# Performance work log

Measured on AMD Instinct MI355X. Metric: run time of the kernel, lower is better.

Reference implementation:

```python
import jax, jax.numpy as jnp
import numpy as np

N_NODES = 100000
N_EDGES = 1000000
NUM_GRAPHS = 100
EPS_BN = 1e-5
EPS_GATE = 1e-6


def _bn(x, gamma, beta):
    # BatchNorm1d in training mode: batch statistics over dim 0
    mu = jnp.mean(x, axis=0)
    var = jnp.var(x, axis=0)
    return (x - mu) * jax.lax.rsqrt(var + EPS_BN) * gamma + beta


def _gated_gcn_layer(h, e, snorm_n, snorm_e, W, b, g_h, b_h, g_e, b_e, src, dst):
    # W: [5, d, d] stacking A, B, C, D, E projections; b: [5, d]
    Ah = h @ W[0] + b[0]
    Bh = h @ W[1] + b[1]
    Ce = e @ W[2] + b[2]
    Dh = h @ W[3] + b[3]
    Eh = h @ W[4] + b[4]
    # edge update: e_ji = Dh_src + Eh_dst + Ce   [E, d]
    e_new = Dh[src] + Eh[dst] + Ce
    sigma = jax.nn.sigmoid(e_new)
    # node update: gated sum of source messages at destination nodes
    num = jax.ops.segment_sum(sigma * Bh[src], dst, num_segments=h.shape[0])
    den = jax.ops.segment_sum(sigma, dst, num_segments=h.shape[0])
    h_new = Ah + num / (den + EPS_GATE)
    # graph size normalization
    h_new = h_new * snorm_n
    e_new = e_new * snorm_e
    # batch norm + relu + residual (dropout = 0.0)
    h_new = jax.nn.relu(_bn(h_new, g_h, b_h))
    e_new = jax.nn.relu(_bn(e_new, g_e, b_e))
    return h + h_new, e + e_new


def setup_inputs() -> dict:
    key = jax.random.key(0)
    ks = jax.random.split(key, 12)
    nodes_feat = jax.random.normal(ks[0], (N_NODES, 64), jnp.float32)
    edges_feat = jax.random.normal(ks[1], (N_EDGES, 1), jnp.float32)
    snorm_n = jax.random.uniform(ks[2], (N_NODES, 1), jnp.float32)
    snorm_e = jax.random.uniform(ks[3], (N_EDGES, 1), jnp.float32)
    src = jax.random.randint(ks[4], (N_EDGES,), 0, N_NODES, jnp.int32)
    dst = jax.random.randint(ks[5], (N_EDGES,), 0, N_NODES, jnp.int32)
    node_graph_ids = jnp.sort(jax.random.randint(ks[6], (N_NODES,), 0, NUM_GRAPHS, jnp.int32))
    Wh = jax.random.normal(ks[7], (64, 70), jnp.float32) * 0.1
    bh = jnp.zeros((70,), jnp.float32)
    We = jax.random.normal(ks[8], (1, 70), jnp.float32) * 0.1
    be = jnp.zeros((70,), jnp.float32)
    W_gcn = jax.random.normal(ks[9], (3, 5, 70, 70), jnp.float32) * 0.1
    b_gcn = jnp.zeros((3, 5, 70), jnp.float32)
    bn_gamma_h = jnp.ones((3, 70), jnp.float32)
    bn_beta_h = jnp.zeros((3, 70), jnp.float32)
    bn_gamma_e = jnp.ones((3, 70), jnp.float32)
    bn_beta_e = jnp.zeros((3, 70), jnp.float32)
    return {"nodes_feat": nodes_feat, "edges_feat": edges_feat, "snorm_n": snorm_n,
            "snorm_e": snorm_e, "src": src, "dst": dst, "node_graph_ids": node_graph_ids,
            "Wh": Wh, "bh": bh, "We": We, "be": be, "W_gcn": W_gcn, "b_gcn": b_gcn,
            "bn_gamma_h": bn_gamma_h, "bn_beta_h": bn_beta_h,
            "bn_gamma_e": bn_gamma_e, "bn_beta_e": bn_beta_e}


def reference(nodes_feat, edges_feat, snorm_n, snorm_e, src, dst, node_graph_ids,
              Wh, bh, We, be, W_gcn, b_gcn, bn_gamma_h, bn_beta_h, bn_gamma_e, bn_beta_e):
    h = nodes_feat @ Wh + bh
    e = edges_feat @ We + be
    # hidden_dims = [70, 70] -> only gated_gcn_1 (params index 0) and gated_gcn_o (index 2)
    for li in (0, 2):
        h, e = _gated_gcn_layer(h, e, snorm_n, snorm_e, W_gcn[li], b_gcn[li],
                                bn_gamma_h[li], bn_beta_h[li], bn_gamma_e[li], bn_beta_e[li],
                                src, dst)
    # dgl.mean_nodes: per-graph mean of node features
    sums = jax.ops.segment_sum(h, node_graph_ids, num_segments=NUM_GRAPHS)
    counts = jax.ops.segment_sum(jnp.ones((h.shape[0],), h.dtype), node_graph_ids,
                                 num_segments=NUM_GRAPHS)
    hg = sums / jnp.maximum(counts, 1.0)[:, None]
    return hg
```

## Files before the change

### kernel.cpp

```cpp
#include <hip/hip_runtime.h>

#define NN 100000
#define NE 1000000
#define NG 100
#define DD 70
#define EL0 64
#define CH0 (9 * EL0)
#define TPW 5
#define EPW (16 * TPW)
#define EPB (4 * EPW)
#define SCB 512
#define WTS (70 * 72)

typedef __attribute__((ext_vector_type(8))) short bf16x8;
typedef __attribute__((ext_vector_type(4))) float f32x4;

__device__ __forceinline__ float sigmoidf_(float x) { return 1.f / (1.f + expf(-x)); }

__device__ __forceinline__ unsigned int rne_bf16(float x) {
    unsigned int u = __float_as_uint(x);
    return (u + 0x7FFFu + ((u >> 16) & 1u)) >> 16;
}
__device__ __forceinline__ float b2f(unsigned short u) {
    return __uint_as_float(((unsigned int)u) << 16);
}

#define DOT4(acc, vv, ww) { acc = fmaf((vv).x, (ww).x, acc); acc = fmaf((vv).y, (ww).y, acc); \
                            acc = fmaf((vv).z, (ww).z, acc); acc = fmaf((vv).w, (ww).w, acc); }

__global__ void k_trAll(const float* __restrict__ Wh, const float* __restrict__ Wg,
                        float* __restrict__ WT) {
    int m = blockIdx.y, f = blockIdx.x, k = threadIdx.x;
    const float* W;
    int K = DD;
    switch (m) {
        case 0: W = Wh; K = 64; break;
        case 1: W = Wg + 0 * 4900; break;
        case 2: W = Wg + 1 * 4900; break;
        case 3: W = Wg + 3 * 4900; break;
        case 4: W = Wg + 4 * 4900; break;
        case 5: W = Wg + 10 * 4900; break;
        case 6: W = Wg + 11 * 4900; break;
        case 7: W = Wg + 13 * 4900; break;
        default: W = Wg + 14 * 4900; break;
    }
    if (k < 72) WT[(m * 70 + f) * 72 + k] = (k < K) ? W[k * DD + f] : 0.f;
}

__global__ __launch_bounds__(640) void k_dense_r(const float* __restrict__ x, int K,
                                                 const float* __restrict__ WTm,
                                                 const float* __restrict__ bias,
                                                 float* __restrict__ out, int nrows) {
    __shared__ float sx[36 * 72];
    int t = threadIdx.x;
    int r = t / DD, f = t - r * DD;
    long rb = (long)blockIdx.x * 36;
    for (int idx = t; idx < 36 * 72; idx += 640) {
        int rr = idx / 72, kk = idx - rr * 72;
        long i = rb + rr;
        sx[idx] = (kk < K && i < nrows) ? x[i * K + kk] : 0.f;
    }
    __syncthreads();
    if (r < 9) {
        const float4* wr = (const float4*)(WTm + f * 72);
        float bb = bias[f];
        float a0 = bb, a1 = bb, a2 = bb, a3 = bb;
        const float4* s0 = (const float4*)&sx[(r) * 72];
        const float4* s1 = (const float4*)&sx[(r + 9) * 72];
        const float4* s2 = (const float4*)&sx[(r + 18) * 72];
        const float4* s3 = (const float4*)&sx[(r + 27) * 72];
#pragma unroll 1
        for (int q = 0; q < 18; q += 2) {
            float4 wA = wr[q], wB = wr[q + 1];
            float4 vA0 = s0[q], vB0 = s0[q + 1];
            DOT4(a0, vA0, wA) DOT4(a0, vB0, wB)
            float4 vA1 = s1[q], vB1 = s1[q + 1];
            DOT4(a1, vA1, wA) DOT4(a1, vB1, wB)
            float4 vA2 = s2[q], vB2 = s2[q + 1];
            DOT4(a2, vA2, wA) DOT4(a2, vB2, wB)
            float4 vA3 = s3[q], vB3 = s3[q + 1];
            DOT4(a3, vA3, wA) DOT4(a3, vB3, wB)
        }
        long i0 = rb + r, i1 = i0 + 9, i2 = i0 + 18, i3 = i0 + 27;
        if (i0 < nrows) out[i0 * DD + f] = a0;
        if (i1 < nrows) out[i1 * DD + f] = a1;
        if (i2 < nrows) out[i2 * DD + f] = a2;
        if (i3 < nrows) out[i3 * DD + f] = a3;
    }
}

#define PROJ(MIDX, BIAS, STORE)                                                   \
    {                                                                             \
        const float4* wr = (const float4*)(WT4 + (MIDX) * WTS + f * 72);          \
        float bb = (BIAS)[f];                                                     \
        float a0 = bb, a1 = bb, a2 = bb, a3 = bb;                                 \
        _Pragma("unroll 1")                                                       \
        for (int q = 0; q < 18; q += 2) {                                         \
            float4 wA = wr[q], wB = wr[q + 1];                                    \
            float4 vA0 = s0[q], vB0 = s0[q + 1];                                  \
            DOT4(a0, vA0, wA) DOT4(a0, vB0, wB)                                   \
            float4 vA1 = s1[q], vB1 = s1[q + 1];                                  \
            DOT4(a1, vA1, wA) DOT4(a1, vB1, wB)                                   \
            float4 vA2 = s2[q], vB2 = s2[q + 1];                                  \
            DOT4(a2, vA2, wA) DOT4(a2, vB2, wB)                                   \
            float4 vA3 = s3[q], vB3 = s3[q + 1];                                  \
            DOT4(a3, vA3, wA) DOT4(a3, vB3, wB)                                   \
        }                                                                         \
        if (i0 < nrows) STORE(i0, a0);                                            \
        if (i1 < nrows) STORE(i1, a1);                                            \
        if (i2 < nrows) STORE(i2, a2);                                            \
        if (i3 < nrows) STORE(i3, a3);                                            \
    }

__global__ __launch_bounds__(640) void k_dense_q(
    const float* __restrict__ x, const float* __restrict__ WT4,
    const float* __restrict__ bA, const float* __restrict__ bB,
    const float* __restrict__ bD, const float* __restrict__ bE,
    float* __restrict__ outA, unsigned short* __restrict__ outB,
    unsigned short* __restrict__ outD, unsigned short* __restrict__ outE, int nrows) {
    __shared__ float sx[36 * 72];
    int t = threadIdx.x;
    int r = t / DD, f = t - r * DD;
    long rb = (long)blockIdx.x * 36;
    for (int idx = t; idx < 36 * 72; idx += 640) {
        int rr = idx / 72, kk = idx - rr * 72;
        long i = rb + rr;
        sx[idx] = (kk < DD && i < nrows) ? x[i * DD + kk] : 0.f;
    }
    __syncthreads();
    if (r < 9) {
        const float4* s0 = (const float4*)&sx[(r) * 72];
        const float4* s1 = (const float4*)&sx[(r + 9) * 72];
        const float4* s2 = (const float4*)&sx[(r + 18) * 72];
        const float4* s3 = (const float4*)&sx[(r + 27) * 72];
        long i0 = rb + r, i1 = i0 + 9, i2 = i0 + 18, i3 = i0 + 27;
#define ST_A(ii, aa) outA[(ii) * DD + f] = (aa)
#define ST_B(ii, aa) outB[(ii) * DD + f] = (unsigned short)rne_bf16(aa)
#define ST_D(ii, aa) outD[(ii) * DD + f] = (unsigned short)rne_bf16(aa)
#define ST_E(ii, aa) outE[(ii) * DD + f] = (unsigned short)rne_bf16(aa)
        PROJ(0, bA, ST_A)
        PROJ(1, bB, ST_B)
        PROJ(2, bD, ST_D)
        PROJ(3, bE, ST_E)
#undef ST_A
#undef ST_B
#undef ST_D
#undef ST_E
    }
}

__global__ void k_pre(const float* __restrict__ We, const float* __restrict__ be,
                      const float* __restrict__ Wg, const float* __restrict__ bg,
                      float* __restrict__ v1, float* __restrict__ v2) {
    int f = threadIdx.x;
    if (f < DD) {
        const float* W2 = Wg + 2 * DD * DD;
        const float* b2 = bg + 2 * DD;
        float a = 0.f, c = 0.f;
        for (int k = 0; k < DD; ++k) {
            a = fmaf(We[k], W2[k * DD + f], a);
            c = fmaf(be[k], W2[k * DD + f], c);
        }
        v1[f] = a;
        v2[f] = c + b2[f];
    }
}

__global__ void k_prep2(const float* __restrict__ v1, const float* __restrict__ v2,
                        const float* __restrict__ murs_e, const float* __restrict__ ge,
                        const float* __restrict__ bbe, const float* __restrict__ We,
                        const float* __restrict__ be, const float* __restrict__ Wg,
                        float* __restrict__ CT2, unsigned short* __restrict__ WB) {
    int t = threadIdx.x;
    if (t < 35) {
        int f0 = 2 * t, f1 = 2 * t + 1;
        float A0 = murs_e[DD + f0] * ge[f0], A1 = murs_e[DD + f1] * ge[f1];
        float* c = CT2 + t * 12;
        c[0] = v1[f0];  c[1] = v1[f1];
        c[2] = v2[f0];  c[3] = v2[f1];
        c[4] = A0;      c[5] = A1;
        c[6] = bbe[f0] - murs_e[f0] * A0;
        c[7] = bbe[f1] - murs_e[f1] * A1;
        c[8] = We[f0];  c[9] = We[f1];
        c[10] = be[f0]; c[11] = be[f1];
    }
    const float* WC2 = Wg + 12 * 4900;
    for (int idx = t; idx < 960; idx += 512) {
        int nt = idx / 192, rem = idx - nt * 192;
        int c = rem / 64, l = rem - c * 64;
        int n = nt * 16 + (l & 15);
        int kb = c * 32 + (l >> 4) * 8;
        for (int j = 0; j < 8; ++j) {
            int k = kb + j;
            unsigned short v = 0;
            if (k < 70 && n < 70) v = (unsigned short)rne_bf16(WC2[k * 70 + n]);
            WB[((nt * 3 + c) * 64 + l) * 8 + j] = v;
        }
    }
}

__global__ void k_count(const int* __restrict__ dst, int* __restrict__ off) {
    int j = blockIdx.x * 256 + threadIdx.x;
    if (j < NE) atomicAdd(&off[dst[j]], 1);
}

__global__ void k_scan_a(int* __restrict__ off, int* __restrict__ part) {
    __shared__ int s[SCB];
    int t = threadIdx.x, i = blockIdx.x * SCB + t;
    int v = (i < NN) ? off[i] : 0;
    s[t] = v;
    __syncthreads();
    for (int d = 1; d < SCB; d <<= 1) {
        int x = (t >= d) ? s[t - d] : 0;
        __syncthreads();
        s[t] += x;
        __syncthreads();
    }
    if (i < NN) off[i] = s[t] - v;
    if (t == SCB - 1) part[blockIdx.x] = s[t];
}

__global__ void k_scan_b(int* __restrict__ part, int nb) {
    __shared__ int s[256];
    int t = threadIdx.x;
    int v = (t < nb) ? part[t] : 0;
    s[t] = v;
    __syncthreads();
    for (int d = 1; d < 256; d <<= 1) {
        int x = (t >= d) ? s[t - d] : 0;
        __syncthreads();
        s[t] += x;
        __syncthreads();
    }
    if (t < nb) part[t] = s[t] - v;
}

__global__ void k_scan_c(int* __restrict__ off, const int* __restrict__ part) {
    int i = blockIdx.x * SCB + threadIdx.x;
    if (i < NN) off[i] += part[blockIdx.x];
}

__global__ void k_fill(const int* __restrict__ src, const int* __restrict__ dst,
                       const float* __restrict__ ef, const float* __restrict__ sne,
                       int* __restrict__ off, int* __restrict__ src_s,
                       float* __restrict__ ef_s, float* __restrict__ sne_s,
                       int* __restrict__ dst_s) {
    int j = blockIdx.x * 256 + threadIdx.x;
    if (j < NE) {
        int d = dst[j];
        int pos = atomicAdd(&off[d], 1);
        src_s[pos] = src[j];
        ef_s[pos] = ef[j];
        sne_s[pos] = sne[j];
        dst_s[pos] = d;
    }
}

__global__ __launch_bounds__(640) void k_edge0(
    const float* __restrict__ ef_s, const float* __restrict__ sne_s,
    const int* __restrict__ src_s, const int* __restrict__ dst_s,
    const unsigned short* __restrict__ PB, const unsigned short* __restrict__ PD,
    const unsigned short* __restrict__ PE, const float* __restrict__ v1,
    const float* __restrict__ v2, float* __restrict__ num,
    float* __restrict__ den, float* __restrict__ red) {
    int t = threadIdx.x;
    int r = t / DD, f = t - r * DD;
    bool act = (r < 9);
    float c1 = 0.f, c2 = 0.f;
    if (act) { c1 = v1[f]; c2 = v2[f]; }
    float acc_s = 0.f, acc_q = 0.f;
    int e_beg = blockIdx.x * CH0 + r * EL0;
    bool live = act && e_beg < NE;
    int dcur = 0;
    float accn = 0.f, accd = 0.f;
    int lim = 0;
    if (live) {
        dcur = dst_s[e_beg];
        lim = NE - e_beg;
        if (lim > EL0) lim = EL0;
    }
    for (int g = 0; g < lim; g += 4) {
        int m = lim - g;
        if (m > 4) m = 4;
        int dj[4];
        float pdj[4], pbj[4], pej[4], efj[4], snj[4];
#pragma unroll
        for (int j = 0; j < 4; ++j) {
            if (j < m) {
                int e = e_beg + g + j;
                int s = src_s[e];
                int d = dst_s[e];
                dj[j] = d;
                efj[j] = ef_s[e];
                snj[j] = sne_s[e];
                pdj[j] = b2f(PD[(long)s * DD + f]);
                pbj[j] = b2f(PB[(long)s * DD + f]);
                pej[j] = b2f(PE[(long)d * DD + f]);
            }
        }
#pragma unroll
        for (int j = 0; j < 4; ++j) {
            if (j < m) {
                if (dj[j] != dcur) {
                    unsafeAtomicAdd(&num[(long)dcur * DD + f], accn);
                    unsafeAtomicAdd(&den[(long)dcur * DD + f], accd);
                    accn = 0.f; accd = 0.f;
                    dcur = dj[j];
                }
                float en = pdj[j] + pej[j] + efj[j] * c1 + c2;
                float sg = sigmoidf_(en);
                accn = fmaf(sg, pbj[j], accn);
                accd += sg;
                float tv = en * snj[j];
                acc_s += tv;
                acc_q = fmaf(tv, tv, acc_q);
            }
        }
    }
    if (live) {
        unsafeAtomicAdd(&num[(long)dcur * DD + f], accn);
        unsafeAtomicAdd(&den[(long)dcur * DD + f], accd);
    }
    __shared__ float ss[DD], sq[DD];
    if (t < DD) { ss[t] = 0.f; sq[t] = 0.f; }
    __syncthreads();
    if (act) { atomicAdd(&ss[f], acc_s); atomicAdd(&sq[f], acc_q); }
    __syncthreads();
    if (t < DD) {
        atomicAdd(&red[t], ss[t]);
        atomicAdd(&red[DD + t], sq[t]);
    }
}

__global__ __launch_bounds__(256) void k_edge2(
    const float* __restrict__ ef_s, const float* __restrict__ sne_s,
    const int* __restrict__ src_s, const int* __restrict__ dst_s,
    const unsigned short* __restrict__ PD0, const unsigned short* __restrict__ PE0,
    const unsigned short* __restrict__ PB2, const unsigned short* __restrict__ PD2,
    const unsigned short* __restrict__ PE2, const float* __restrict__ CT2,
    const unsigned short* __restrict__ WB, const float* __restrict__ bC2,
    float* __restrict__ num, float* __restrict__ den) {
    __shared__ __align__(16) unsigned short As[4 * 16 * 104];
    int t = threadIdx.x;
    int w = t >> 6, l = t & 63;
    unsigned short* Aw = &As[w * 1664];
    for (int i = l; i < 832; i += 64) ((unsigned int*)Aw)[i] = 0u;
    int wb_e = blockIdx.x * EPB + w * EPW;
    if (wb_e >= NE) return;
    int col = l & 15, hi = l >> 4;
    bf16x8 bfr[15];
#pragma unroll
    for (int q = 0; q < 15; ++q)
        bfr[q] = *(const bf16x8*)(WB + (q * 64 + l) * 8);
    float bc[5];
#pragma unroll
    for (int nt = 0; nt < 5; ++nt) bc[nt] = bC2[nt * 16 + col];
    int e0p = wb_e + hi * 4;
    if (e0p > NE - 1) e0p = NE - 1;
    int dcur = dst_s[e0p];
    float an[5], ad[5];
#pragma unroll
    for (int nt = 0; nt < 5; ++nt) { an[nt] = 0.f; ad[nt] = 0.f; }
    for (int tt = 0; tt < TPW; ++tt) {
        int et = wb_e + tt * 16;
        if (et >= NE) break;
        for (int i = l; i < 560; i += 64) {
            int el = i / 35, fp = i - el * 35, f = fp * 2;
            int e = et + el;
            unsigned int val = 0u;
            if (e < NE) {
                int s = src_s[e], d = dst_s[e];
                float efv = ef_s[e], sn = sne_s[e];
                const float* ct = CT2 + fp * 12;
                unsigned int upd = *(const unsigned int*)(PD0 + (long)s * DD + f);
                unsigned int upe = *(const unsigned int*)(PE0 + (long)d * DD + f);
                float pdx = __uint_as_float(upd << 16);
                float pdy = __uint_as_float(upd & 0xFFFF0000u);
                float pex = __uint_as_float(upe << 16);
                float pey = __uint_as_float(upe & 0xFFFF0000u);
                float en0a = pdx + pex + efv * ct[0] + ct[2];
                float en0b = pdy + pey + efv * ct[1] + ct[3];
                float ra = fmaxf(fmaf(en0a * sn, ct[4], ct[6]), 0.f);
                float rb = fmaxf(fmaf(en0b * sn, ct[5], ct[7]), 0.f);
                float e1a = fmaf(efv, ct[8], ct[10]) + ra;
                float e1b = fmaf(efv, ct[9], ct[11]) + rb;
                val = rne_bf16(e1a) | (rne_bf16(e1b) << 16);
            }
            ((unsigned int*)Aw)[(el * 104 + f) >> 1] = val;
        }
        bf16x8 af[3];
#pragma unroll
        for (int c = 0; c < 3; ++c)
            af[c] = *(const bf16x8*)(Aw + (l & 15) * 104 + c * 32 + hi * 8);
        f32x4 acc[5];
#pragma unroll
        for (int nt = 0; nt < 5; ++nt) {
            acc[nt] = (f32x4){0.f, 0.f, 0.f, 0.f};
#pragma unroll
            for (int c = 0; c < 3; ++c)
                acc[nt] = __builtin_amdgcn_mfma_f32_16x16x32_bf16(af[c], bfr[nt * 3 + c],
                                                                  acc[nt], 0, 0, 0);
        }
#pragma unroll
        for (int j = 0; j < 4; ++j) {
            int e = et + hi * 4 + j;
            if (e < NE) {
                int d = dst_s[e];
                if (d != dcur) {
#pragma unroll
                    for (int nt = 0; nt < 5; ++nt) {
                        int nv = nt * 16 + col;
                        if (nv < 70) {
                            unsafeAtomicAdd(&num[(long)dcur * DD + nv], an[nt]);
                            unsafeAtomicAdd(&den[(long)dcur * DD + nv], ad[nt]);
                        }
                        an[nt] = 0.f; ad[nt] = 0.f;
                    }
                    dcur = d;
                }
                int s = src_s[e];
#pragma unroll
                for (int nt = 0; nt < 5; ++nt) {
                    int nv = nt * 16 + col;
                    if (nv < 70) {
                        float en = acc[nt][j] + bc[nt] + b2f(PD2[(long)s * DD + nv])
                                 + b2f(PE2[(long)d * DD + nv]);
                        float sg = sigmoidf_(en);
                        an[nt] = fmaf(sg, b2f(PB2[(long)s * DD + nv]), an[nt]);
                        ad[nt] += sg;
                    }
                }
            }
        }
    }
#pragma unroll
    for (int nt = 0; nt < 5; ++nt) {
        int nv = nt * 16 + col;
        if (nv < 70) {
            unsafeAtomicAdd(&num[(long)dcur * DD + nv], an[nt]);
            unsafeAtomicAdd(&den[(long)dcur * DD + nv], ad[nt]);
        }
    }
}

__global__ __launch_bounds__(640) void k_nstats(const float* __restrict__ PA,
                                                const float* __restrict__ num,
                                                const float* __restrict__ den,
                                                const float* __restrict__ snn,
                                                float* __restrict__ red) {
    int t = threadIdx.x;
    int r = t / DD, f = t - r * DD;
    bool act = (r < 9);
    float acc_s = 0.f, acc_q = 0.f;
    const int T = (NN + 8) / 9;
    for (int tile = blockIdx.x; tile < T; tile += gridDim.x) {
        int i = tile * 9 + r;
        if (act && i < NN) {
            long o = (long)i * DD + f;
            float v = (PA[o] + num[o] / (den[o] + 1e-6f)) * snn[i];
            acc_s += v;
            acc_q = fmaf(v, v, acc_q);
        }
    }
    __shared__ float ss[DD], sq[DD];
    if (t < DD) { ss[t] = 0.f; sq[t] = 0.f; }
    __syncthreads();
    if (act) { atomicAdd(&ss[f], acc_s); atomicAdd(&sq[f], acc_q); }
    __syncthreads();
    if (t < DD) {
        atomicAdd(&red[t], ss[t]);
        atomicAdd(&red[DD + t], sq[t]);
    }
}

__global__ void k_stats(const float* __restrict__ sums, float* __restrict__ murs, float invn) {
    int f = threadIdx.x;
    if (f < DD) {
        float mu = sums[f] * invn;
        float var = sums[DD + f] * invn - mu * mu;
        murs[f] = mu;
        murs[DD + f] = rsqrtf(var + 1e-5f);
    }
}

__global__ __launch_bounds__(256) void k_apply(const float* __restrict__ hin,
                                               const float* __restrict__ PA,
                                               const float* __restrict__ num,
                                               const float* __restrict__ den,
                                               const float* __restrict__ snn,
                                               const float* __restrict__ murs,
                                               const float* __restrict__ g,
                                               const float* __restrict__ b,
                                               float* __restrict__ hout) {
    long idx = (long)blockIdx.x * 256 + threadIdx.x;
    if (idx < (long)NN * DD) {
        int i = (int)(idx / DD);
        int f = (int)(idx - (long)i * DD);
        float v = (PA[idx] + num[idx] / (den[idx] + 1e-6f)) * snn[i];
        float bnv = (v - murs[f]) * murs[DD + f] * g[f] + b[f];
        hout[idx] = hin[idx] + fmaxf(bnv, 0.f);
    }
}

__global__ __launch_bounds__(640) void k_readout(const float* __restrict__ h,
                                                 const int* __restrict__ gid,
                                                 float* __restrict__ gsum,
                                                 float* __restrict__ gcnt) {
    __shared__ float sv[9 * DD];
    __shared__ int sg_[9];
    int t = threadIdx.x;
    int r = t / DD, f = t - r * DD;
    int i = blockIdx.x * 9 + r;
    if (r < 9 && i < NN) {
        sv[r * DD + f] = h[(long)i * DD + f];
        if (f == 0) sg_[r] = gid[i];
    }
    __syncthreads();
    int nvalid = NN - blockIdx.x * 9;
    if (nvalid > 9) nvalid = 9;
    if (t < DD && nvalid > 0) {
        float acc = 0.f;
        int cur = sg_[0];
        for (int rr = 0; rr < nvalid; ++rr) {
            int g = sg_[rr];
            if (g != cur) {
                unsafeAtomicAdd(&gsum[cur * DD + t], acc);
                acc = 0.f;
                cur = g;
            }
            acc += sv[rr * DD + t];
        }
        unsafeAtomicAdd(&gsum[cur * DD + t], acc);
        if (t == 0) {
            int cnt = 0;
            cur = sg_[0];
            for (int rr = 0; rr < nvalid; ++rr) {
                if (sg_[rr] != cur) {
                    unsafeAtomicAdd(&gcnt[cur], (float)cnt);
                    cnt = 0;
                    cur = sg_[rr];
                }
                cnt++;
            }
            unsafeAtomicAdd(&gcnt[cur], (float)cnt);
        }
    }
}

__global__ void k_out(const float* __restrict__ gsum, const float* __restrict__ gcnt,
                      float* __restrict__ out) {
    int idx = blockIdx.x * 256 + threadIdx.x;
    if (idx < NG * DD) {
        int g = idx / DD;
        out[idx] = gsum[idx] / fmaxf(gcnt[g], 1.f);
    }
}

extern "C" void kernel_launch(void* const* d_in, const int* in_sizes, int n_in,
                              void* d_out, int out_size, void* d_ws, size_t ws_size,
                              hipStream_t stream) {
    const float* x   = (const float*)d_in[0];
    const float* ef  = (const float*)d_in[1];
    const float* snn = (const float*)d_in[2];
    const float* sne = (const float*)d_in[3];
    const int*   src = (const int*)d_in[4];
    const int*   dst = (const int*)d_in[5];
    const int*   gid = (const int*)d_in[6];
    const float* Wh  = (const float*)d_in[7];
    const float* bh  = (const float*)d_in[8];
    const float* We  = (const float*)d_in[9];
    const float* be  = (const float*)d_in[10];
    const float* Wg  = (const float*)d_in[11];
    const float* bg  = (const float*)d_in[12];
    const float* gh  = (const float*)d_in[13];
    const float* bbh = (const float*)d_in[14];
    const float* ge  = (const float*)d_in[15];
    const float* bbe = (const float*)d_in[16];
    float* out = (float*)d_out;

    const size_t NF = (size_t)NN * DD;

    float* ws = (float*)d_ws;
    float* B0 = ws;
    float* B1 = B0 + NF;
    float* B2 = B1 + NF;
    float* B3 = B2 + NF;
    float* B4 = B3 + NF;
    float* B5 = B4 + NF;
    float* B6 = B5 + NF;
    float* num = B6 + NF;
    float* den = num + NF;
    float* red  = den + NF;
    float* gsum = red + 4 * DD;
    float* gcnt = gsum + NG * DD;
    float* v1 = gcnt + NG;
    float* v2 = v1 + DD;
    float* murs_e = v2 + DD;
    float* murs_h = murs_e + 2 * DD;
    int* src_s = (int*)(murs_h + 2 * DD);
    float* ef_s  = (float*)(src_s + NE);
    float* sne_s = ef_s + NE;
    int* dst_s = (int*)(sne_s + NE);
    float* WT    = (float*)(dst_s + NE);
    uintptr_t pal = ((uintptr_t)(WT + 10 * WTS) + 15) & ~(uintptr_t)15;
    float* CT2 = (float*)pal;
    unsigned short* WB = (unsigned short*)(CT2 + 420);
    int* off  = (int*)num;
    int* part = off + NN;

    unsigned short* B0h = (unsigned short*)B0;
    unsigned short* B3h = (unsigned short*)B3;
    unsigned short* B4h = (unsigned short*)B4;
    unsigned short* B5h = (unsigned short*)B5;
    unsigned short* B6h = (unsigned short*)B6;

    size_t need = (size_t)((char*)(WB + 7680) - (char*)d_ws);
    if (ws_size < need) return;

    const int NB_N36 = (NN + 35) / 36;
    const int NB_N9  = (NN + 8) / 9;
    const int NB_E256 = (NE + 255) / 256;
    const int NB_SC  = (NN + SCB - 1) / SCB;
    const int NB_E0  = (NE + CH0 - 1) / CH0;
    const int NB_E2  = (NE + EPB - 1) / EPB;

    hipMemsetAsync(off, 0, NN * sizeof(int), stream);
    k_trAll<<<dim3(70, 9), 72, 0, stream>>>(Wh, Wg, WT);
    k_count<<<NB_E256, 256, 0, stream>>>(dst, off);
    k_scan_a<<<NB_SC, SCB, 0, stream>>>(off, part);
    k_scan_b<<<1, 256, 0, stream>>>(part, NB_SC);
    k_scan_c<<<NB_SC, SCB, 0, stream>>>(off, part);
    k_fill<<<NB_E256, 256, 0, stream>>>(src, dst, ef, sne, off, src_s, ef_s, sne_s, dst_s);

    hipMemsetAsync(num, 0, (2 * NF + 4 * DD + NG * DD + NG) * sizeof(float), stream);

    k_pre<<<1, 128, 0, stream>>>(We, be, Wg, bg, v1, v2);
    k_dense_r<<<NB_N36, 640, 0, stream>>>(x, 64, WT + 0 * WTS, bh, B0, NN);

    k_dense_q<<<NB_N36, 640, 0, stream>>>(B0, WT + 1 * WTS, bg + 0 * 70, bg + 1 * 70,
                                          bg + 3 * 70, bg + 4 * 70, B2, B3h, B4h, B5h, NN);
    k_edge0<<<NB_E0, 640, 0, stream>>>(ef_s, sne_s, src_s, dst_s, B3h, B4h, B5h, v1, v2,
                                       num, den, red);
    k_stats<<<1, 128, 0, stream>>>(red, murs_e, 1.f / NE);
    k_prep2<<<1, 512, 0, stream>>>(v1, v2, murs_e, ge + 0, bbe + 0, We, be, Wg, CT2, WB);
    k_nstats<<<2048, 640, 0, stream>>>(B2, num, den, snn, red + 2 * DD);
    k_stats<<<1, 128, 0, stream>>>(red + 2 * DD, murs_h, 1.f / NN);
    k_apply<<<(int)((NF + 255) / 256), 256, 0, stream>>>(B0, B2, num, den, snn, murs_h,
                                                         gh + 0, bbh + 0, B1);

    hipMemsetAsync(num, 0, (2 * NF + 4 * DD) * sizeof(float), stream);
    k_dense_q<<<NB_N36, 640, 0, stream>>>(B1, WT + 5 * WTS, bg + 10 * 70, bg + 11 * 70,
                                          bg + 13 * 70, bg + 14 * 70, B2, B3h, B0h, B6h, NN);
    k_edge2<<<NB_E2, 256, 0, stream>>>(ef_s, sne_s, src_s, dst_s, B4h, B5h, B3h, B0h, B6h,
                                       CT2, WB, bg + 12 * 70, num, den);
    k_nstats<<<2048, 640, 0, stream>>>(B2, num, den, snn, red + 2 * DD);
    k_stats<<<1, 128, 0, stream>>>(red + 2 * DD, murs_h, 1.f / NN);
    k_apply<<<(int)((NF + 255) / 256), 256, 0, stream>>>(B1, B2, num, den, snn, murs_h,
                                                         gh + 2 * DD, bbh + 2 * DD, B1);

    k_readout<<<NB_N9, 640, 0, stream>>>(B1, gid, gsum, gcnt);
    k_out<<<(NG * DD + 255) / 256, 256, 0, stream>>>(gsum, gcnt, out);
}
```

Measured before the change: 1.707 ms.

## Interleave Dh and Bh as packed bf16 pairs and cache Eh per destination

The dense projection kernel now writes Dh and Bh for each node as one packed 32-bit word, so each edge kernel fetches both source-gathered values with one load instead of two. Because edges are sorted by destination, both edge kernels load Eh[dst] only when the destination changes rather than on every edge. This cuts random gather traffic in the edge-heavy kernels. In exchange, buffer roles are reassigned, and the dense kernel still writes a separate Dh array that later layers reuse, so node-side writes grow somewhat.

```diff
diff --git a/kernel.cpp b/kernel.cpp
--- a/kernel.cpp
+++ b/kernel.cpp
@@ -24,6 +24,8 @@
 __device__ __forceinline__ float b2f(unsigned short u) {
     return __uint_as_float(((unsigned int)u) << 16);
 }
+__device__ __forceinline__ float lo2f(unsigned int u) { return __uint_as_float(u << 16); }
+__device__ __forceinline__ float hi2f(unsigned int u) { return __uint_as_float(u & 0xFFFF0000u); }
 
 #define DOT4(acc, vv, ww) { acc = fmaf((vv).x, (ww).x, acc); acc = fmaf((vv).y, (ww).y, acc); \
                             acc = fmaf((vv).z, (ww).z, acc); acc = fmaf((vv).w, (ww).w, acc); }
@@ -106,18 +108,18 @@
             float4 vA3 = s3[q], vB3 = s3[q + 1];                                  \
             DOT4(a3, vA3, wA) DOT4(a3, vB3, wB)                                   \
         }                                                                         \
-        if (i0 < nrows) STORE(i0, a0);                                            \
-        if (i1 < nrows) STORE(i1, a1);                                            \
-        if (i2 < nrows) STORE(i2, a2);                                            \
-        if (i3 < nrows) STORE(i3, a3);                                            \
+        STORE(0, i0, a0)                                                          \
+        STORE(1, i1, a1)                                                          \
+        STORE(2, i2, a2)                                                          \
+        STORE(3, i3, a3)                                                          \
     }
 
 __global__ __launch_bounds__(640) void k_dense_q(
     const float* __restrict__ x, const float* __restrict__ WT4,
     const float* __restrict__ bA, const float* __restrict__ bB,
     const float* __restrict__ bD, const float* __restrict__ bE,
-    float* __restrict__ outA, unsigned short* __restrict__ outB,
-    unsigned short* __restrict__ outD, unsigned short* __restrict__ outE, int nrows) {
+    float* __restrict__ outA, unsigned short* __restrict__ outDstd,
+    unsigned short* __restrict__ outE, unsigned int* __restrict__ outDB, int nrows) {
     __shared__ float sx[36 * 72];
     int t = threadIdx.x;
     int r = t / DD, f = t - r * DD;
@@ -134,10 +136,13 @@
         const float4* s2 = (const float4*)&sx[(r + 18) * 72];
         const float4* s3 = (const float4*)&sx[(r + 27) * 72];
         long i0 = rb + r, i1 = i0 + 9, i2 = i0 + 18, i3 = i0 + 27;
-#define ST_A(ii, aa) outA[(ii) * DD + f] = (aa)
-#define ST_B(ii, aa) outB[(ii) * DD + f] = (unsigned short)rne_bf16(aa)
-#define ST_D(ii, aa) outD[(ii) * DD + f] = (unsigned short)rne_bf16(aa)
-#define ST_E(ii, aa) outE[(ii) * DD + f] = (unsigned short)rne_bf16(aa)
+        float vB0 = 0.f, vB1 = 0.f, vB2 = 0.f, vB3 = 0.f;
+#define ST_A(row, ii, aa) if ((ii) < nrows) outA[(ii) * DD + f] = (aa);
+#define ST_B(row, ii, aa) vB##row = (aa);
+#define ST_D(row, ii, aa) if ((ii) < nrows) { unsigned int ud = rne_bf16(aa); \
+            outDstd[(ii) * DD + f] = (unsigned short)ud; \
+            outDB[(ii) * DD + f] = ud | (rne_bf16(vB##row) << 16); }
+#define ST_E(row, ii, aa) if ((ii) < nrows) outE[(ii) * DD + f] = (unsigned short)rne_bf16(aa);
         PROJ(0, bA, ST_A)
         PROJ(1, bB, ST_B)
         PROJ(2, bD, ST_D)
@@ -259,10 +264,9 @@
 __global__ __launch_bounds__(640) void k_edge0(
     const float* __restrict__ ef_s, const float* __restrict__ sne_s,
     const int* __restrict__ src_s, const int* __restrict__ dst_s,
-    const unsigned short* __restrict__ PB, const unsigned short* __restrict__ PD,
-    const unsigned short* __restrict__ PE, const float* __restrict__ v1,
-    const float* __restrict__ v2, float* __restrict__ num,
-    float* __restrict__ den, float* __restrict__ red) {
+    const unsigned int* __restrict__ DB0, const unsigned short* __restrict__ PE,
+    const float* __restrict__ v1, const float* __restrict__ v2,
+    float* __restrict__ num, float* __restrict__ den, float* __restrict__ red) {
     int t = threadIdx.x;
     int r = t / DD, f = t - r * DD;
     bool act = (r < 9);
@@ -272,10 +276,11 @@
     int e_beg = blockIdx.x * CH0 + r * EL0;
     bool live = act && e_beg < NE;
     int dcur = 0;
-    float accn = 0.f, accd = 0.f;
+    float pe = 0.f, accn = 0.f, accd = 0.f;
     int lim = 0;
     if (live) {
         dcur = dst_s[e_beg];
+        pe = b2f(PE[(long)dcur * DD + f]);
         lim = NE - e_beg;
         if (lim > EL0) lim = EL0;
     }
@@ -283,19 +288,17 @@
         int m = lim - g;
         if (m > 4) m = 4;
         int dj[4];
-        float pdj[4], pbj[4], pej[4], efj[4], snj[4];
+        unsigned int dbj[4];
+        float efj[4], snj[4];
 #pragma unroll
         for (int j = 0; j < 4; ++j) {
             if (j < m) {
                 int e = e_beg + g + j;
                 int s = src_s[e];
-                int d = dst_s[e];
-                dj[j] = d;
+                dj[j] = dst_s[e];
                 efj[j] = ef_s[e];
                 snj[j] = sne_s[e];
-                pdj[j] = b2f(PD[(long)s * DD + f]);
-                pbj[j] = b2f(PB[(long)s * DD + f]);
-                pej[j] = b2f(PE[(long)d * DD + f]);
+                dbj[j] = DB0[(long)s * DD + f];
             }
         }
 #pragma unroll
@@ -306,10 +309,11 @@
                     unsafeAtomicAdd(&den[(long)dcur * DD + f], accd);
                     accn = 0.f; accd = 0.f;
                     dcur = dj[j];
+                    pe = b2f(PE[(long)dcur * DD + f]);
                 }
-                float en = pdj[j] + pej[j] + efj[j] * c1 + c2;
+                float en = lo2f(dbj[j]) + pe + efj[j] * c1 + c2;
                 float sg = sigmoidf_(en);
-                accn = fmaf(sg, pbj[j], accn);
+                accn = fmaf(sg, hi2f(dbj[j]), accn);
                 accd += sg;
                 float tv = en * snj[j];
                 acc_s += tv;
@@ -336,10 +340,9 @@
     const float* __restrict__ ef_s, const float* __restrict__ sne_s,
     const int* __restrict__ src_s, const int* __restrict__ dst_s,
     const unsigned short* __restrict__ PD0, const unsigned short* __restrict__ PE0,
-    const unsigned short* __restrict__ PB2, const unsigned short* __restrict__ PD2,
-    const unsigned short* __restrict__ PE2, const float* __restrict__ CT2,
-    const unsigned short* __restrict__ WB, const float* __restrict__ bC2,
-    float* __restrict__ num, float* __restrict__ den) {
+    const unsigned int* __restrict__ DB2, const unsigned short* __restrict__ PE2,
+    const float* __restrict__ CT2, const unsigned short* __restrict__ WB,
+    const float* __restrict__ bC2, float* __restrict__ num, float* __restrict__ den) {
     __shared__ __align__(16) unsigned short As[4 * 16 * 104];
     int t = threadIdx.x;
     int w = t >> 6, l = t & 63;
@@ -358,9 +361,13 @@
     int e0p = wb_e + hi * 4;
     if (e0p > NE - 1) e0p = NE - 1;
     int dcur = dst_s[e0p];
-    float an[5], ad[5];
-#pragma unroll
-    for (int nt = 0; nt < 5; ++nt) { an[nt] = 0.f; ad[nt] = 0.f; }
+    float an[5], ad[5], pe2c[5];
+#pragma unroll
+    for (int nt = 0; nt < 5; ++nt) {
+        an[nt] = 0.f; ad[nt] = 0.f;
+        int nv = nt * 16 + col;
+        pe2c[nt] = (nv < 70) ? b2f(PE2[(long)dcur * DD + nv]) : 0.f;
+    }
     for (int tt = 0; tt < TPW; ++tt) {
         int et = wb_e + tt * 16;
         if (et >= NE) break;
@@ -374,10 +381,8 @@
                 const float* ct = CT2 + fp * 12;
                 unsigned int upd = *(const unsigned int*)(PD0 + (long)s * DD + f);
                 unsigned int upe = *(const unsigned int*)(PE0 + (long)d * DD + f);
-                float pdx = __uint_as_float(upd << 16);
-                float pdy = __uint_as_float(upd & 0xFFFF0000u);
-                float pex = __uint_as_float(upe << 16);
-                float pey = __uint_as_float(upe & 0xFFFF0000u);
+                float pdx = lo2f(upd), pdy = hi2f(upd);
+                float pex = lo2f(upe), pey = hi2f(upe);
                 float en0a = pdx + pex + efv * ct[0] + ct[2];
                 float en0b = pdy + pey + efv * ct[1] + ct[3];
                 float ra = fmaxf(fmaf(en0a * sn, ct[4], ct[6]), 0.f);
@@ -417,16 +422,21 @@
                         an[nt] = 0.f; ad[nt] = 0.f;
                     }
                     dcur = d;
+#pragma unroll
+                    for (int nt = 0; nt < 5; ++nt) {
+                        int nv = nt * 16 + col;
+                        if (nv < 70) pe2c[nt] = b2f(PE2[(long)dcur * DD + nv]);
+                    }
                 }
                 int s = src_s[e];
 #pragma unroll
                 for (int nt = 0; nt < 5; ++nt) {
                     int nv = nt * 16 + col;
                     if (nv < 70) {
-                        float en = acc[nt][j] + bc[nt] + b2f(PD2[(long)s * DD + nv])
-                                 + b2f(PE2[(long)d * DD + nv]);
+                        unsigned int db = DB2[(long)s * DD + nv];
+                        float en = acc[nt][j] + bc[nt] + lo2f(db) + pe2c[nt];
                         float sg = sigmoidf_(en);
-                        an[nt] = fmaf(sg, b2f(PB2[(long)s * DD + nv]), an[nt]);
+                        an[nt] = fmaf(sg, hi2f(db), an[nt]);
                         ad[nt] += sg;
                     }
                 }
@@ -608,11 +618,12 @@
     int* off  = (int*)num;
     int* part = off + NN;
 
-    unsigned short* B0h = (unsigned short*)B0;
     unsigned short* B3h = (unsigned short*)B3;
     unsigned short* B4h = (unsigned short*)B4;
     unsigned short* B5h = (unsigned short*)B5;
     unsigned short* B6h = (unsigned short*)B6;
+    unsigned int*   B6u = (unsigned int*)B6;
+    unsigned int*   B0u = (unsigned int*)B0;
 
     size_t need = (size_t)((char*)(WB + 7680) - (char*)d_ws);
     if (ws_size < need) return;
@@ -638,8 +649,8 @@
     k_dense_r<<<NB_N36, 640, 0, stream>>>(x, 64, WT + 0 * WTS, bh, B0, NN);
 
     k_dense_q<<<NB_N36, 640, 0, stream>>>(B0, WT + 1 * WTS, bg + 0 * 70, bg + 1 * 70,
-                                          bg + 3 * 70, bg + 4 * 70, B2, B3h, B4h, B5h, NN);
-    k_edge0<<<NB_E0, 640, 0, stream>>>(ef_s, sne_s, src_s, dst_s, B3h, B4h, B5h, v1, v2,
+                                          bg + 3 * 70, bg + 4 * 70, B2, B4h, B5h, B6u, NN);
+    k_edge0<<<NB_E0, 640, 0, stream>>>(ef_s, sne_s, src_s, dst_s, B6u, B5h, v1, v2,
                                        num, den, red);
     k_stats<<<1, 128, 0, stream>>>(red, murs_e, 1.f / NE);
     k_prep2<<<1, 512, 0, stream>>>(v1, v2, murs_e, ge + 0, bbe + 0, We, be, Wg, CT2, WB);
@@ -650,8 +661,8 @@
 
     hipMemsetAsync(num, 0, (2 * NF + 4 * DD) * sizeof(float), stream);
     k_dense_q<<<NB_N36, 640, 0, stream>>>(B1, WT + 5 * WTS, bg + 10 * 70, bg + 11 * 70,
-                                          bg + 13 * 70, bg + 14 * 70, B2, B3h, B0h, B6h, NN);
-    k_edge2<<<NB_E2, 256, 0, stream>>>(ef_s, sne_s, src_s, dst_s, B4h, B5h, B3h, B0h, B6h,
+                                          bg + 13 * 70, bg + 14 * 70, B2, B3h, B6h, B0u, NN);
+    k_edge2<<<NB_E2, 256, 0, stream>>>(ef_s, sne_s, src_s, dst_s, B4h, B5h, B0u, B6h,
                                        CT2, WB, bg + 12 * 70, num, den);
     k_nstats<<<2048, 640, 0, stream>>>(B2, num, den, snn, red + 2 * DD);
     k_stats<<<1, 128, 0, stream>>>(red + 2 * DD, murs_h, 1.f / NN);
```

After: 1.583 ms. 1.08x faster.
